# Performance work log

Hardware: AMD Instinct MI355X
Metric: run time of the kernel (lower is better)

## Reference

```python
import jax, jax.numpy as jnp
import numpy as np

B, S, D, H = 2, 2048, 1024, 16  # batch, seq_len, d_model(=d_k=d_v), heads
HD = D // H                      # per-head dim = 64


def setup_inputs() -> dict:
    key = jax.random.key(0)
    ks = jax.random.split(key, 7)
    s = 0.02  # weight init scale
    return {
        "queries": jax.random.normal(ks[0], (B, S, D), dtype=jnp.float32),
        "keys":    jax.random.normal(ks[1], (B, S, D), dtype=jnp.float32),
        "values":  jax.random.normal(ks[2], (B, S, D), dtype=jnp.float32),
        "Wq": jax.random.normal(ks[3], (D, D), dtype=jnp.float32) * s,
        "bq": jnp.zeros((D,), dtype=jnp.float32),
        "Wk": jax.random.normal(ks[4], (D, D), dtype=jnp.float32) * s,
        "bk": jnp.zeros((D,), dtype=jnp.float32),
        "Wv": jax.random.normal(ks[5], (D, D), dtype=jnp.float32) * s,
        "bv": jnp.zeros((D,), dtype=jnp.float32),
        "Wo": jax.random.normal(ks[6], (D, D), dtype=jnp.float32) * s,
        "bo": jnp.zeros((D,), dtype=jnp.float32),
    }


def reference(queries, keys, values, Wq, bq, Wk, bk, Wv, bv, Wo, bo):
    def split_heads(x):  # [B,S,D] -> [B,H,S,HD]
        return x.reshape(B, S, H, HD).transpose(0, 2, 1, 3)

    q = split_heads(queries @ Wq + bq)
    k = split_heads(keys @ Wk + bk)
    v = split_heads(values @ Wv + bv)

    # NOTE: original module scales by sqrt(total d_k = D), not per-head dim.
    scores = jnp.einsum('bhqd,bhkd->bhqk', q, k) / jnp.sqrt(jnp.float32(D))
    weights = jax.nn.softmax(scores, axis=-1)
    o = jnp.einsum('bhqk,bhkd->bhqd', weights, v)

    o = o.transpose(0, 2, 1, 3).reshape(B, S, D)  # merge heads
    return o @ Wo + bo
```

## Files before the change

### kernel.cpp

```cpp
#include <hip/hip_runtime.h>
#include <hip/hip_bf16.h>
#include <stdint.h>

#define S_LEN 2048
#define D_MOD 1024
#define NHEAD 16
#define BATCH 2
#define M_TOT (BATCH * S_LEN)

typedef __bf16 bf16_t;
typedef __bf16 bf16x8 __attribute__((ext_vector_type(8)));
typedef __bf16 bf16x4 __attribute__((ext_vector_type(4)));
typedef float f32x4 __attribute__((ext_vector_type(4)));

typedef __attribute__((address_space(1))) void gas_void;
typedef __attribute__((address_space(3))) void las_void;

__device__ __forceinline__ void gload_lds16(const void* g, void* l) {
#if defined(__has_builtin) && __has_builtin(__builtin_amdgcn_global_load_lds)
  __builtin_amdgcn_global_load_lds((gas_void*)g, (las_void*)l, 16u, 0, 0u);
#else
  *(bf16x8*)l = *(const bf16x8*)g;
#endif
}

__device__ __forceinline__ f32x4 mfma16(bf16x8 a, bf16x8 b, f32x4 c) {
  return __builtin_amdgcn_mfma_f32_16x16x32_bf16(a, b, c, 0, 0, 0);
}

__global__ __launch_bounds__(256) void cvt3_kernel(
    const float* __restrict__ a, const float* __restrict__ b, const float* __restrict__ c,
    bf16_t* __restrict__ oa, bf16_t* __restrict__ ob, bf16_t* __restrict__ oc)
{
  const float* in  = blockIdx.z == 0 ? a : (blockIdx.z == 1 ? b : c);
  bf16_t*      out = blockIdx.z == 0 ? oa : (blockIdx.z == 1 ? ob : oc);
  int i = blockIdx.x * 256 + threadIdx.x;
  float4 v = ((const float4*)in)[i];
  bf16x4 o;
  o[0] = (bf16_t)v.x; o[1] = (bf16_t)v.y; o[2] = (bf16_t)v.z; o[3] = (bf16_t)v.w;
  ((bf16x4*)out)[i] = o;
}

__global__ __launch_bounds__(256) void wtrans_kernel(
    const float* __restrict__ w0, const float* __restrict__ w1,
    const float* __restrict__ w2, const float* __restrict__ w3,
    bf16_t* __restrict__ t0, bf16_t* __restrict__ t1,
    bf16_t* __restrict__ t2, bf16_t* __restrict__ t3)
{
  __shared__ float tile[64][65];
  const int z = blockIdx.z;
  const float* W = z == 0 ? w0 : (z == 1 ? w1 : (z == 2 ? w2 : w3));
  bf16_t* Wt     = z == 0 ? t0 : (z == 1 ? t1 : (z == 2 ? t2 : t3));
  const int tid = threadIdx.x;
  const int kb = blockIdx.y * 64, nb = blockIdx.x * 64;
#pragma unroll
  for (int j = 0; j < 16; j++) {
    int flat = j * 256 + tid;
    int kr = flat >> 6, nc = flat & 63;
    tile[kr][nc] = W[(size_t)(kb + kr) * D_MOD + nb + nc];
  }
  __syncthreads();
#pragma unroll
  for (int j = 0; j < 16; j++) {
    int flat = j * 256 + tid;
    int nr = flat >> 6, kc = flat & 63;
    Wt[(size_t)(nb + nr) * D_MOD + kb + kc] = (bf16_t)tile[kc][nr];
  }
}

__device__ __forceinline__ void gemm_core(const bf16_t* __restrict__ A,
                                          const bf16_t* __restrict__ Bt,
                                          bf16_t* As, bf16_t* Bs,
                                          int mbase, int nbase, f32x4 acc[4][4])
{
  const int tid = threadIdx.x;
  const int lane = tid & 63, wave = tid >> 6;
  const int lrow = lane & 15, lg = lane >> 4;
  const int wm = wave >> 1, wn = wave & 1;
  const int rs = lrow & 7;

  auto stage = [&](int buf, int kt) {
#pragma unroll
    for (int j = 0; j < 4; j++) {
      int flat = j * 256 + tid;
      int r = flat >> 3, c8 = flat & 7;
      int sc8 = c8 ^ (r & 7);
      gload_lds16(A  + (size_t)(mbase + r) * D_MOD + kt + sc8 * 8, As + buf * 8192 + flat * 8);
      gload_lds16(Bt + (size_t)(nbase + r) * D_MOD + kt + sc8 * 8, Bs + buf * 8192 + flat * 8);
    }
  };

  stage(0, 0);
  __syncthreads();

  for (int kt = 0; kt < D_MOD; kt += 64) {
    const int cur = (kt >> 6) & 1;
    if (kt + 64 < D_MOD) stage(cur ^ 1, kt + 64);
    const bf16_t* Ac = As + cur * 8192;
    const bf16_t* Bc = Bs + cur * 8192;
#pragma unroll
    for (int kc = 0; kc < 2; kc++) {
      bf16x8 af[4], bfr[4];
#pragma unroll
      for (int mt = 0; mt < 4; mt++)
        af[mt] = *(const bf16x8*)(Ac + (wm * 64 + mt * 16 + lrow) * 64 + ((kc * 4 + lg) ^ rs) * 8);
#pragma unroll
      for (int nt = 0; nt < 4; nt++)
        bfr[nt] = *(const bf16x8*)(Bc + (wn * 64 + nt * 16 + lrow) * 64 + ((kc * 4 + lg) ^ rs) * 8);
      __builtin_amdgcn_s_setprio(1);
#pragma unroll
      for (int mt = 0; mt < 4; mt++)
#pragma unroll
        for (int nt = 0; nt < 4; nt++)
          acc[mt][nt] = mfma16(af[mt], bfr[nt], acc[mt][nt]);
      __builtin_amdgcn_s_setprio(0);
    }
    __syncthreads();
  }
}

__global__ __launch_bounds__(256) void gemm_qkv_kernel(
    const bf16_t* __restrict__ Xq, const bf16_t* __restrict__ Xk, const bf16_t* __restrict__ Xv,
    const bf16_t* __restrict__ WqT, const bf16_t* __restrict__ WkT, const bf16_t* __restrict__ WvT,
    const float* __restrict__ bq, const float* __restrict__ bk, const float* __restrict__ bv,
    bf16_t* __restrict__ Qp, bf16_t* __restrict__ Kp, bf16_t* __restrict__ Vt)
{
  __shared__ __align__(16) bf16_t As[2 * 128 * 64];
  __shared__ __align__(16) bf16_t Bs[2 * 128 * 64];
  const int z = blockIdx.z;
  const bf16_t* A    = z == 0 ? Xq  : (z == 1 ? Xk  : Xv);
  const bf16_t* Bt   = z == 0 ? WqT : (z == 1 ? WkT : WvT);
  const float*  bias = z == 0 ? bq  : (z == 1 ? bk  : bv);
  f32x4 acc[4][4] = {};
  const int mbase = blockIdx.y * 128, nbase = blockIdx.x * 128;
  gemm_core(A, Bt, As, Bs, mbase, nbase, acc);
  const int tid = threadIdx.x, lane = tid & 63, wave = tid >> 6;
  const int lrow = lane & 15, lg = lane >> 4, wm = wave >> 1, wn = wave & 1;
  if (z < 2) {
    bf16_t* Out = z == 0 ? Qp : Kp;
#pragma unroll
    for (int mt = 0; mt < 4; mt++) {
      int r0 = mbase + wm * 64 + mt * 16 + lg * 4;
#pragma unroll
      for (int nt = 0; nt < 4; nt++) {
        int col = nbase + wn * 64 + nt * 16 + lrow;
        float bb = bias[col];
#pragma unroll
        for (int r = 0; r < 4; r++)
          Out[(size_t)(r0 + r) * D_MOD + col] = (bf16_t)(acc[mt][nt][r] + bb);
      }
    }
  } else {
#pragma unroll
    for (int mt = 0; mt < 4; mt++) {
      int r0 = mbase + wm * 64 + mt * 16 + lg * 4;
      int b = r0 >> 11, s0 = r0 & (S_LEN - 1);
#pragma unroll
      for (int nt = 0; nt < 4; nt++) {
        int col = nbase + wn * 64 + nt * 16 + lrow;
        float bb = bias[col];
        bf16x4 pk;
#pragma unroll
        for (int r = 0; r < 4; r++) pk[r] = (bf16_t)(acc[mt][nt][r] + bb);
        *(bf16x4*)(Vt + ((size_t)(b * NHEAD + (col >> 6)) * 64 + (col & 63)) * S_LEN + s0) = pk;
      }
    }
  }
}

__global__ __launch_bounds__(256) void attn_kernel(
    const bf16_t* __restrict__ Q, const bf16_t* __restrict__ K,
    const bf16_t* __restrict__ Vt, bf16_t* __restrict__ O)
{
  __shared__ __align__(16) bf16_t Ks[2][64 * 64];
  __shared__ __align__(16) bf16_t Vs[2][64 * 64];
  __shared__ __align__(16) bf16_t plds[4][32 * 72];
  const int tid = threadIdx.x, wave = tid >> 6, lane = tid & 63;
  const int lrow = lane & 15, lg = lane >> 4;
  const int bh = blockIdx.y;
  const int b = bh >> 4, h = bh & 15;
  const int qbase = blockIdx.x * 128 + wave * 32;
  const bf16_t* Kb = K + (size_t)(b * S_LEN) * D_MOD + h * 64;
  const bf16_t* Vb = Vt + (size_t)bh * 64 * S_LEN;

  bf16x8 qf[2][2];
#pragma unroll
  for (int qr = 0; qr < 2; qr++) {
    const bf16_t* Qrow = Q + (size_t)(b * S_LEN + qbase + qr * 16 + lrow) * D_MOD + h * 64;
    qf[qr][0] = *(const bf16x8*)(Qrow + lg * 8);
    qf[qr][1] = *(const bf16x8*)(Qrow + 32 + lg * 8);
  }

  float mrow[2] = {-1e30f, -1e30f};
  float lsum[2] = {0.f, 0.f};
  f32x4 oacc[2][4] = {};

  bf16_t* pl = (bf16_t*)plds[wave];
  const float sc2 = 0.03125f * 1.44269504f;
  const int rs = lrow & 7;

  auto stage = [&](int buf, int kt) {
#pragma unroll
    for (int j = 0; j < 2; j++) {
      int flat = j * 256 + tid;
      int r = flat >> 3, c8 = flat & 7;
      int sc8 = c8 ^ (r & 7);
      gload_lds16(Kb + (size_t)(kt + r) * D_MOD + sc8 * 8, &Ks[buf][flat * 8]);
    }
#pragma unroll
    for (int j = 0; j < 2; j++) {
      int flat = j * 256 + tid;
      int r = flat >> 3, c8 = flat & 7;
      int sc8 = c8 ^ (r & 7);
      gload_lds16(Vb + (size_t)r * S_LEN + kt + sc8 * 8, &Vs[buf][flat * 8]);
    }
  };

  stage(0, 0);
  __syncthreads();

  for (int kt = 0; kt < S_LEN; kt += 64) {
    const int cur = (kt >> 6) & 1;
    if (kt + 64 < S_LEN) stage(cur ^ 1, kt + 64);
    const bf16_t* Kc = Ks[cur];
    const bf16_t* Vc = Vs[cur];

    bf16x8 kf[4][2];
#pragma unroll
    for (int ct = 0; ct < 4; ct++) {
      int row = ct * 16 + lrow;
      kf[ct][0] = *(const bf16x8*)(Kc + row * 64 + ((lg) ^ rs) * 8);
      kf[ct][1] = *(const bf16x8*)(Kc + row * 64 + ((4 + lg) ^ rs) * 8);
    }
    f32x4 st[2][4] = {};
    __builtin_amdgcn_s_setprio(1);
#pragma unroll
    for (int qr = 0; qr < 2; qr++)
#pragma unroll
      for (int ct = 0; ct < 4; ct++) {
        st[qr][ct] = mfma16(kf[ct][0], qf[qr][0], st[qr][ct]);
        st[qr][ct] = mfma16(kf[ct][1], qf[qr][1], st[qr][ct]);
      }
    __builtin_amdgcn_s_setprio(0);

    float corr_pv[2][4];
#pragma unroll
    for (int qr = 0; qr < 2; qr++) {
      f32x4 m01, m23, mm;
#pragma unroll
      for (int r = 0; r < 4; r++) {
        m01[r] = fmaxf(st[qr][0][r], st[qr][1][r]);
        m23[r] = fmaxf(st[qr][2][r], st[qr][3][r]);
        mm[r] = fmaxf(m01[r], m23[r]);
      }
      float rmax = fmaxf(fmaxf(mm[0], mm[1]), fmaxf(mm[2], mm[3]));
      rmax = fmaxf(rmax, __shfl_xor(rmax, 16));
      rmax = fmaxf(rmax, __shfl_xor(rmax, 32));
      float mn = fmaxf(mrow[qr], rmax * sc2);
      float corr = __builtin_amdgcn_exp2f(mrow[qr] - mn);
      mrow[qr] = mn;
      f32x4 p[4];
      f32x4 ps;
#pragma unroll
      for (int r = 0; r < 4; r++) {
        p[0][r] = __builtin_amdgcn_exp2f(__builtin_fmaf(st[qr][0][r], sc2, -mn));
        p[1][r] = __builtin_amdgcn_exp2f(__builtin_fmaf(st[qr][1][r], sc2, -mn));
        p[2][r] = __builtin_amdgcn_exp2f(__builtin_fmaf(st[qr][2][r], sc2, -mn));
        p[3][r] = __builtin_amdgcn_exp2f(__builtin_fmaf(st[qr][3][r], sc2, -mn));
        ps[r] = (p[0][r] + p[1][r]) + (p[2][r] + p[3][r]);
      }
      float rsum = (ps[0] + ps[1]) + (ps[2] + ps[3]);
      rsum += __shfl_xor(rsum, 16);
      rsum += __shfl_xor(rsum, 32);
      lsum[qr] = lsum[qr] * corr + rsum;
#pragma unroll
      for (int ct = 0; ct < 4; ct++) {
        bf16x4 pk;
#pragma unroll
        for (int r = 0; r < 4; r++) pk[r] = (bf16_t)p[ct][r];
        *(bf16x4*)(pl + (qr * 16 + lrow) * 72 + ct * 16 + lg * 4) = pk;
      }
#pragma unroll
      for (int r = 0; r < 4; r++)
        corr_pv[qr][r] = __shfl(corr, lg * 4 + r);
    }
#pragma unroll
    for (int qr = 0; qr < 2; qr++)
#pragma unroll
      for (int nt = 0; nt < 4; nt++)
#pragma unroll
        for (int r = 0; r < 4; r++)
          oacc[qr][nt][r] *= corr_pv[qr][r];

    bf16x8 vf[4][2];
#pragma unroll
    for (int nt = 0; nt < 4; nt++) {
      int row = nt * 16 + lrow;
      vf[nt][0] = *(const bf16x8*)(Vc + row * 64 + ((lg) ^ rs) * 8);
      vf[nt][1] = *(const bf16x8*)(Vc + row * 64 + ((4 + lg) ^ rs) * 8);
    }
    __builtin_amdgcn_s_setprio(1);
#pragma unroll
    for (int qr = 0; qr < 2; qr++)
#pragma unroll
      for (int kc = 0; kc < 2; kc++) {
        bf16x8 af = *(const bf16x8*)(pl + (qr * 16 + lrow) * 72 + kc * 32 + lg * 8);
#pragma unroll
        for (int nt = 0; nt < 4; nt++)
          oacc[qr][nt] = mfma16(af, vf[nt][kc], oacc[qr][nt]);
      }
    __builtin_amdgcn_s_setprio(0);

    __syncthreads();
  }

  bf16_t* Or = O + (size_t)(b * S_LEN + qbase) * D_MOD + h * 64;
#pragma unroll
  for (int qr = 0; qr < 2; qr++) {
    float linv[4];
#pragma unroll
    for (int r = 0; r < 4; r++)
      linv[r] = 1.f / __shfl(lsum[qr], lg * 4 + r);
#pragma unroll
    for (int r = 0; r < 4; r++)
#pragma unroll
      for (int nt = 0; nt < 4; nt++)
        Or[(size_t)(qr * 16 + lg * 4 + r) * D_MOD + nt * 16 + lrow] = (bf16_t)(oacc[qr][nt][r] * linv[r]);
  }
}

__global__ __launch_bounds__(256) void gemm_o_kernel(
    const bf16_t* __restrict__ A, const bf16_t* __restrict__ Bt,
    const float* __restrict__ bias, float* __restrict__ Out)
{
  __shared__ __align__(16) bf16_t As[2 * 128 * 64];
  __shared__ __align__(16) bf16_t Bs[2 * 128 * 64];
  f32x4 acc[4][4] = {};
  const int mbase = blockIdx.y * 128, nbase = blockIdx.x * 128;
  gemm_core(A, Bt, As, Bs, mbase, nbase, acc);
  const int tid = threadIdx.x, lane = tid & 63, wave = tid >> 6;
  const int lrow = lane & 15, lg = lane >> 4, wm = wave >> 1, wn = wave & 1;
#pragma unroll
  for (int mt = 0; mt < 4; mt++) {
    int r0 = mbase + wm * 64 + mt * 16 + lg * 4;
#pragma unroll
    for (int nt = 0; nt < 4; nt++) {
      int col = nbase + wn * 64 + nt * 16 + lrow;
      float bb = bias[col];
#pragma unroll
      for (int r = 0; r < 4; r++)
        Out[(size_t)(r0 + r) * D_MOD + col] = acc[mt][nt][r] + bb;
    }
  }
}

extern "C" void kernel_launch(void* const* d_in, const int* in_sizes, int n_in,
                              void* d_out, int out_size, void* d_ws, size_t ws_size,
                              hipStream_t stream) {
  const float* q  = (const float*)d_in[0];
  const float* k  = (const float*)d_in[1];
  const float* v  = (const float*)d_in[2];
  const float* Wq = (const float*)d_in[3];
  const float* bq = (const float*)d_in[4];
  const float* Wk = (const float*)d_in[5];
  const float* bk = (const float*)d_in[6];
  const float* Wv = (const float*)d_in[7];
  const float* bv = (const float*)d_in[8];
  const float* Wo = (const float*)d_in[9];
  const float* bo = (const float*)d_in[10];
  float* out = (float*)d_out;

  char* ws = (char*)d_ws;
  const size_t MB = 1024 * 1024;
  bf16_t* Xq  = (bf16_t*)(ws + 0 * MB);
  bf16_t* Xk  = (bf16_t*)(ws + 8 * MB);
  bf16_t* Xv  = (bf16_t*)(ws + 16 * MB);
  bf16_t* WqT = (bf16_t*)(ws + 24 * MB);
  bf16_t* WkT = (bf16_t*)(ws + 26 * MB);
  bf16_t* WvT = (bf16_t*)(ws + 28 * MB);
  bf16_t* WoT = (bf16_t*)(ws + 30 * MB);
  bf16_t* Qp  = (bf16_t*)(ws + 32 * MB);
  bf16_t* Kp  = (bf16_t*)(ws + 40 * MB);
  bf16_t* Vt  = (bf16_t*)(ws + 48 * MB);
  bf16_t* AO  = (bf16_t*)(ws + 0 * MB);

  dim3 cb(256);
  cvt3_kernel<<<dim3(4096, 1, 3), cb, 0, stream>>>(q, k, v, Xq, Xk, Xv);
  wtrans_kernel<<<dim3(16, 16, 4), cb, 0, stream>>>(Wq, Wk, Wv, Wo, WqT, WkT, WvT, WoT);
  gemm_qkv_kernel<<<dim3(8, 32, 3), cb, 0, stream>>>(Xq, Xk, Xv, WqT, WkT, WvT,
                                                     bq, bk, bv, Qp, Kp, Vt);
  attn_kernel<<<dim3(16, 32), cb, 0, stream>>>(Qp, Kp, Vt, AO);
  gemm_o_kernel<<<dim3(8, 32), cb, 0, stream>>>(AO, WoT, bo, out);
}
```

Measured before the change: 260.9 us.

## Fuse fp32-to-bf16 input conversion into QKV GEMM A-tile staging

Removes the separate cvt3 kernel and has the QKV GEMM read fp32 activations directly into registers, convert them to bf16, and write them swizzled into LDS, prefetching one tile ahead. This avoids writing and re-reading three 8 MB bf16 copies plus one launch. In exchange, the A tile no longer uses async global-to-LDS loads: it doubles global read bytes per tile and holds more registers, which may hurt GEMM occupancy or overlap. gemm_core is inlined into the O-projection kernel unchanged.

```diff
diff --git a/kernel.cpp b/kernel.cpp
--- a/kernel.cpp
+++ b/kernel.cpp
@@ -26,19 +26,6 @@
 
 __device__ __forceinline__ f32x4 mfma16(bf16x8 a, bf16x8 b, f32x4 c) {
   return __builtin_amdgcn_mfma_f32_16x16x32_bf16(a, b, c, 0, 0, 0);
-}
-
-__global__ __launch_bounds__(256) void cvt3_kernel(
-    const float* __restrict__ a, const float* __restrict__ b, const float* __restrict__ c,
-    bf16_t* __restrict__ oa, bf16_t* __restrict__ ob, bf16_t* __restrict__ oc)
-{
-  const float* in  = blockIdx.z == 0 ? a : (blockIdx.z == 1 ? b : c);
-  bf16_t*      out = blockIdx.z == 0 ? oa : (blockIdx.z == 1 ? ob : oc);
-  int i = blockIdx.x * 256 + threadIdx.x;
-  float4 v = ((const float4*)in)[i];
-  bf16x4 o;
-  o[0] = (bf16_t)v.x; o[1] = (bf16_t)v.y; o[2] = (bf16_t)v.z; o[3] = (bf16_t)v.w;
-  ((bf16x4*)out)[i] = o;
 }
 
 __global__ __launch_bounds__(256) void wtrans_kernel(
@@ -68,59 +55,8 @@
   }
 }
 
-__device__ __forceinline__ void gemm_core(const bf16_t* __restrict__ A,
-                                          const bf16_t* __restrict__ Bt,
-                                          bf16_t* As, bf16_t* Bs,
-                                          int mbase, int nbase, f32x4 acc[4][4])
-{
-  const int tid = threadIdx.x;
-  const int lane = tid & 63, wave = tid >> 6;
-  const int lrow = lane & 15, lg = lane >> 4;
-  const int wm = wave >> 1, wn = wave & 1;
-  const int rs = lrow & 7;
-
-  auto stage = [&](int buf, int kt) {
-#pragma unroll
-    for (int j = 0; j < 4; j++) {
-      int flat = j * 256 + tid;
-      int r = flat >> 3, c8 = flat & 7;
-      int sc8 = c8 ^ (r & 7);
-      gload_lds16(A  + (size_t)(mbase + r) * D_MOD + kt + sc8 * 8, As + buf * 8192 + flat * 8);
-      gload_lds16(Bt + (size_t)(nbase + r) * D_MOD + kt + sc8 * 8, Bs + buf * 8192 + flat * 8);
-    }
-  };
-
-  stage(0, 0);
-  __syncthreads();
-
-  for (int kt = 0; kt < D_MOD; kt += 64) {
-    const int cur = (kt >> 6) & 1;
-    if (kt + 64 < D_MOD) stage(cur ^ 1, kt + 64);
-    const bf16_t* Ac = As + cur * 8192;
-    const bf16_t* Bc = Bs + cur * 8192;
-#pragma unroll
-    for (int kc = 0; kc < 2; kc++) {
-      bf16x8 af[4], bfr[4];
-#pragma unroll
-      for (int mt = 0; mt < 4; mt++)
-        af[mt] = *(const bf16x8*)(Ac + (wm * 64 + mt * 16 + lrow) * 64 + ((kc * 4 + lg) ^ rs) * 8);
-#pragma unroll
-      for (int nt = 0; nt < 4; nt++)
-        bfr[nt] = *(const bf16x8*)(Bc + (wn * 64 + nt * 16 + lrow) * 64 + ((kc * 4 + lg) ^ rs) * 8);
-      __builtin_amdgcn_s_setprio(1);
-#pragma unroll
-      for (int mt = 0; mt < 4; mt++)
-#pragma unroll
-        for (int nt = 0; nt < 4; nt++)
-          acc[mt][nt] = mfma16(af[mt], bfr[nt], acc[mt][nt]);
-      __builtin_amdgcn_s_setprio(0);
-    }
-    __syncthreads();
-  }
-}
-
 __global__ __launch_bounds__(256) void gemm_qkv_kernel(
-    const bf16_t* __restrict__ Xq, const bf16_t* __restrict__ Xk, const bf16_t* __restrict__ Xv,
+    const float* __restrict__ Xq, const float* __restrict__ Xk, const float* __restrict__ Xv,
     const bf16_t* __restrict__ WqT, const bf16_t* __restrict__ WkT, const bf16_t* __restrict__ WvT,
     const float* __restrict__ bq, const float* __restrict__ bk, const float* __restrict__ bv,
     bf16_t* __restrict__ Qp, bf16_t* __restrict__ Kp, bf16_t* __restrict__ Vt)
@@ -128,14 +64,87 @@
   __shared__ __align__(16) bf16_t As[2 * 128 * 64];
   __shared__ __align__(16) bf16_t Bs[2 * 128 * 64];
   const int z = blockIdx.z;
-  const bf16_t* A    = z == 0 ? Xq  : (z == 1 ? Xk  : Xv);
+  const float*  A    = z == 0 ? Xq  : (z == 1 ? Xk  : Xv);
   const bf16_t* Bt   = z == 0 ? WqT : (z == 1 ? WkT : WvT);
   const float*  bias = z == 0 ? bq  : (z == 1 ? bk  : bv);
+
+  const int tid = threadIdx.x;
+  const int lane = tid & 63, wave = tid >> 6;
+  const int lrow = lane & 15, lg = lane >> 4;
+  const int wm = wave >> 1, wn = wave & 1;
+  const int rs = lrow & 7;
+  const int mbase = blockIdx.y * 128, nbase = blockIdx.x * 128;
   f32x4 acc[4][4] = {};
-  const int mbase = blockIdx.y * 128, nbase = blockIdx.x * 128;
-  gemm_core(A, Bt, As, Bs, mbase, nbase, acc);
-  const int tid = threadIdx.x, lane = tid & 63, wave = tid >> 6;
-  const int lrow = lane & 15, lg = lane >> 4, wm = wave >> 1, wn = wave & 1;
+
+  int srow[4], sc8x[4];
+#pragma unroll
+  for (int j = 0; j < 4; j++) {
+    int flat = j * 256 + tid;
+    srow[j] = flat >> 3;
+    sc8x[j] = (flat & 7) ^ (srow[j] & 7);
+  }
+
+  auto loadA = [&](f32x4 (&a0)[4], f32x4 (&a1)[4], int kt) {
+#pragma unroll
+    for (int j = 0; j < 4; j++) {
+      const float* src = A + (size_t)(mbase + srow[j]) * D_MOD + kt + sc8x[j] * 8;
+      a0[j] = *(const f32x4*)src;
+      a1[j] = *(const f32x4*)(src + 4);
+    }
+  };
+  auto writeA = [&](int buf, f32x4 (&a0)[4], f32x4 (&a1)[4]) {
+#pragma unroll
+    for (int j = 0; j < 4; j++) {
+      int flat = j * 256 + tid;
+      bf16x8 o;
+#pragma unroll
+      for (int e = 0; e < 4; e++) { o[e] = (bf16_t)a0[j][e]; o[4 + e] = (bf16_t)a1[j][e]; }
+      *(bf16x8*)(As + buf * 8192 + flat * 8) = o;
+    }
+  };
+  auto stageB = [&](int buf, int kt) {
+#pragma unroll
+    for (int j = 0; j < 4; j++)
+      gload_lds16(Bt + (size_t)(nbase + srow[j]) * D_MOD + kt + sc8x[j] * 8,
+                  Bs + buf * 8192 + (j * 256 + tid) * 8);
+  };
+
+  f32x4 a0[4], a1[4];
+  loadA(a0, a1, 0);
+  stageB(0, 0);
+  writeA(0, a0, a1);
+  __syncthreads();
+
+  for (int kt = 0; kt < D_MOD; kt += 64) {
+    const int cur = (kt >> 6) & 1;
+    const bool nxt = (kt + 64 < D_MOD);
+    if (nxt) {
+      loadA(a0, a1, kt + 64);
+      stageB(cur ^ 1, kt + 64);
+    }
+    const bf16_t* Ac = As + cur * 8192;
+    const bf16_t* Bc = Bs + cur * 8192;
+#pragma unroll
+    for (int kc = 0; kc < 2; kc++) {
+      bf16x8 af[4], bfr[4];
+#pragma unroll
+      for (int mt = 0; mt < 4; mt++)
+        af[mt] = *(const bf16x8*)(Ac + (wm * 64 + mt * 16 + lrow) * 64 + ((kc * 4 + lg) ^ rs) * 8);
+#pragma unroll
+      for (int nt = 0; nt < 4; nt++)
+        bfr[nt] = *(const bf16x8*)(Bc + (wn * 64 + nt * 16 + lrow) * 64 + ((kc * 4 + lg) ^ rs) * 8);
+      __builtin_amdgcn_s_setprio(1);
+#pragma unroll
+      for (int mt = 0; mt < 4; mt++)
+#pragma unroll
+        for (int nt = 0; nt < 4; nt++)
+          acc[mt][nt] = mfma16(af[mt], bfr[nt], acc[mt][nt]);
+      __builtin_amdgcn_s_setprio(0);
+    }
+    if (nxt) writeA(cur ^ 1, a0, a1);
+    __syncthreads();
+  }
+
   if (z < 2) {
     bf16_t* Out = z == 0 ? Qp : Kp;
 #pragma unroll
@@ -335,11 +344,55 @@
 {
   __shared__ __align__(16) bf16_t As[2 * 128 * 64];
   __shared__ __align__(16) bf16_t Bs[2 * 128 * 64];
+  const int tid = threadIdx.x;
+  const int lane = tid & 63, wave = tid >> 6;
+  const int lrow = lane & 15, lg = lane >> 4;
+  const int wm = wave >> 1, wn = wave & 1;
+  const int rs = lrow & 7;
+  const int mbase = blockIdx.y * 128, nbase = blockIdx.x * 128;
   f32x4 acc[4][4] = {};
-  const int mbase = blockIdx.y * 128, nbase = blockIdx.x * 128;
-  gemm_core(A, Bt, As, Bs, mbase, nbase, acc);
-  const int tid = threadIdx.x, lane = tid & 63, wave = tid >> 6;
-  const int lrow = lane & 15, lg = lane >> 4, wm = wave >> 1, wn = wave & 1;
+
+  auto stage = [&](int buf, int kt) {
+#pragma unroll
+    for (int j = 0; j < 4; j++) {
+      int flat = j * 256 + tid;
+      int r = flat >> 3, c8 = flat & 7;
+      int sc8 = c8 ^ (r & 7);
+      gload_lds16(A  + (size_t)(mbase + r) * D_MOD + kt + sc8 * 8, As + buf * 8192 + flat * 8);
+      gload_lds16(Bt + (size_t)(nbase + r) * D_MOD + kt + sc8 * 8, Bs + buf * 8192 + flat * 8);
+    }
+  };
+
+  stage(0, 0);
+  __syncthreads();
+
+  for (int kt = 0; kt < D_MOD; kt += 64) {
+    const int cur = (kt >> 6) & 1;
+    if (kt + 64 < D_MOD) stage(cur ^ 1, kt + 64);
+    const bf16_t* Ac = As + cur * 8192;
+    const bf16_t* Bc = Bs + cur * 8192;
+#pragma unroll
+    for (int kc = 0; kc < 2; kc++) {
+      bf16x8 af[4], bfr[4];
+#pragma unroll
+      for (int mt = 0; mt < 4; mt++)
+        af[mt] = *(const bf16x8*)(Ac + (wm * 64 + mt * 16 + lrow) * 64 + ((kc * 4 + lg) ^ rs) * 8);
+#pragma unroll
+      for (int nt = 0; nt < 4; nt++)
+        bfr[nt] = *(const bf16x8*)(Bc + (wn * 64 + nt * 16 + lrow) * 64 + ((kc * 4 + lg) ^ rs) * 8);
+      __builtin_amdgcn_s_setprio(1);
+#pragma unroll
+      for (int mt = 0; mt < 4; mt++)
+#pragma unroll
+        for (int nt = 0; nt < 4; nt++)
+          acc[mt][nt] = mfma16(af[mt], bfr[nt], acc[mt][nt]);
+      __builtin_amdgcn_s_setprio(0);
+    }
+    __syncthreads();
+  }
+
+  const int lane2 = tid & 63;
+  (void)lane2;
 #pragma unroll
   for (int mt = 0; mt < 4; mt++) {
     int r0 = mbase + wm * 64 + mt * 16 + lg * 4;
@@ -372,9 +425,7 @@
 
   char* ws = (char*)d_ws;
   const size_t MB = 1024 * 1024;
-  bf16_t* Xq  = (bf16_t*)(ws + 0 * MB);
-  bf16_t* Xk  = (bf16_t*)(ws + 8 * MB);
-  bf16_t* Xv  = (bf16_t*)(ws + 16 * MB);
+  bf16_t* AO  = (bf16_t*)(ws + 0 * MB);
   bf16_t* WqT = (bf16_t*)(ws + 24 * MB);
   bf16_t* WkT = (bf16_t*)(ws + 26 * MB);
   bf16_t* WvT = (bf16_t*)(ws + 28 * MB);
@@ -382,12 +433,10 @@
   bf16_t* Qp  = (bf16_t*)(ws + 32 * MB);
   bf16_t* Kp  = (bf16_t*)(ws + 40 * MB);
   bf16_t* Vt  = (bf16_t*)(ws + 48 * MB);
-  bf16_t* AO  = (bf16_t*)(ws + 0 * MB);
 
   dim3 cb(256);
-  cvt3_kernel<<<dim3(4096, 1, 3), cb, 0, stream>>>(q, k, v, Xq, Xk, Xv);
   wtrans_kernel<<<dim3(16, 16, 4), cb, 0, stream>>>(Wq, Wk, Wv, Wo, WqT, WkT, WvT, WoT);
-  gemm_qkv_kernel<<<dim3(8, 32, 3), cb, 0, stream>>>(Xq, Xk, Xv, WqT, WkT, WvT,
+  gemm_qkv_kernel<<<dim3(8, 32, 3), cb, 0, stream>>>(q, k, v, WqT, WkT, WvT,
                                                      bq, bk, bv, Qp, Kp, Vt);
   attn_kernel<<<dim3(16, 32), cb, 0, stream>>>(Qp, Kp, Vt, AO);
   gemm_o_kernel<<<dim3(8, 32), cb, 0, stream>>>(AO, WoT, bo, out);
```

Result: slower. 269.8 us (+3.4%).
